# Optimization experiments

Measured on AMD Instinct MI355X. Metric: run time of the kernel, lower is better.

## Reference

```python
import jax, jax.numpy as jnp
import numpy as np

SIZE = 128  # matches init_kwargs output_shape
EPS = 1e-12  # numerical floor for 1 - sum_of_squares (original TF code has none; values stay >0 analytically)


def _chol_from_z(zvec):
    """Build lower-triangular Cholesky factor of a correlation matrix from
    canonical partial-correlation parameters z (|z|<1), per batch row.
    Column j: zeros above, diag = sqrt(1 - s[j]), below-diag = z[i,j]*sqrt(1 - s[i]),
    where s accumulates the row-wise sum of squares of previous columns.
    """
    B = zvec.shape[0]
    n = SIZE
    rows, cols = np.tril_indices(n, -1)  # strictly lower triangle, row-major (matches l_indices)
    z = jnp.zeros((B, n, n), zvec.dtype).at[:, rows, cols].set(zvec)  # [B,n,n]
    i = jnp.arange(n)

    def step(s, xs):
        zcol, j = xs                      # zcol: [B,n] = z[:, :, j]
        sq = jnp.sqrt(jnp.clip(1.0 - s, EPS))  # [B,n] = sqrt(1 - running sum of squares)
        col = jnp.where(i == j, sq, jnp.where(i > j, zcol * sq, 0.0))
        return s + col * col, col

    s0 = jnp.zeros((B, n), zvec.dtype)
    _, cols_out = jax.lax.scan(step, s0, (jnp.moveaxis(z, 2, 0), i))  # cols_out: [n(col), B, n(row)]
    return jnp.transpose(cols_out, (1, 2, 0))  # [B, n, n], L[b, row, col]


def setup_inputs() -> dict:
    key = jax.random.key(0)
    B = 2048
    nz = SIZE * (SIZE - 1) // 2  # 8128
    # canonical partial correlations must lie in (-1, 1)
    zvec = jax.random.uniform(key, (B, nz), jnp.float32, -0.9, 0.9)
    return {"inputs": zvec}


def reference(inputs):
    return _chol_from_z(inputs)
```

## Files before the change

kernel.cpp:

```cpp
#include <hip/hip_runtime.h>

#define NROW 128
#define NZ   8128
#define EPSF 1e-12f
#define RPW  8

typedef float vfloat2 __attribute__((ext_vector_type(2)));

#define DPP_MUL(x, ctrl, rmask)                                               \
  x *= __int_as_float(__builtin_amdgcn_update_dpp(                            \
      0x3f800000, __float_as_int(x), ctrl, rmask, 0xF, false))

__global__ __launch_bounds__(256) void chol_from_z_kernel(
    const float* __restrict__ z, float* __restrict__ out)
{
    const int gtid = blockIdx.x * blockDim.x + threadIdx.x;
    const int w    = gtid >> 6;
    const int lane = threadIdx.x & 63;

    const int row0 = w * RPW;
    const int b    = row0 >> 7;
    const float* __restrict__ zb = z + (size_t)b * NZ;

    const int p0 = lane << 1;
    const int p1 = p0 | 1;

    float zA[RPW], zB[RPW];
    #pragma unroll
    for (int k = 0; k < RPW; ++k) {
        const int i    = (row0 + k) & 127;
        const int base = (i * (i - 1)) >> 1;
        const int ap   = base + p0;
        const int a    = min(ap, NZ - 2);
        const float2 v = *reinterpret_cast<const float2*>(zb + a);
        zA[k] = (ap > a) ? v.y : v.x;
        zB[k] = v.y;
    }

    #pragma unroll
    for (int k = 0; k < RPW; ++k) {
        const int  i  = (row0 + k) & 127;
        const bool m0 = (p0 < i);
        const bool m1 = (p1 < i);
        const float z0 = zA[k], z1 = zB[k];

        const float f0   = m0 ? fmaf(-z0, z0, 1.0f) : 1.0f;
        const float f1   = m1 ? fmaf(-z1, z1, 1.0f) : 1.0f;
        const float pair = f0 * f1;

        float x = pair;
        DPP_MUL(x, 0x111, 0xF);
        DPP_MUL(x, 0x112, 0xF);
        DPP_MUL(x, 0x114, 0xF);
        DPP_MUL(x, 0x118, 0xF);
        DPP_MUL(x, 0x142, 0xA);
        DPP_MUL(x, 0x143, 0xC);

        const float e    = x * __builtin_amdgcn_rcpf(pair);
        const float pre1 = e * f0;

        const float sq0 = __builtin_amdgcn_sqrtf(fmaxf(e,    EPSF));
        const float sq1 = __builtin_amdgcn_sqrtf(fmaxf(pre1, EPSF));

        const float o0 = m0 ? z0 * sq0 : ((p0 == i) ? sq0 : 0.0f);
        const float o1 = m1 ? z1 * sq1 : ((p1 == i) ? sq1 : 0.0f);

        vfloat2 v; v.x = o0; v.y = o1;
        vfloat2* dst = reinterpret_cast<vfloat2*>(out + (size_t)(row0 + k) * NROW + p0);
        __builtin_nontemporal_store(v, dst);
    }
}

extern "C" void kernel_launch(void* const* d_in, const int* in_sizes, int n_in,
                              void* d_out, int out_size, void* d_ws, size_t ws_size,
                              hipStream_t stream)
{
    const float* z = (const float*)d_in[0];
    float* out = (float*)d_out;

    const int B = in_sizes[0] / NZ;
    const int nrows_total = B * NROW;
    const int nwaves = nrows_total / RPW;

    const int block = 256;
    const int grid = (nwaves * 64) / block;
    chol_from_z_kernel<<<grid, block, 0, stream>>>(z, out);
}
```

Baseline: 36.06 us.

## Process four row-units per wave with double-buffered software-pipelined loads

Each wave now handles four 8-row units spaced a grid stride apart instead of one. Loads for the next unit are issued before the current unit is computed and stored, ping-ponging between two register buffers so memory latency overlaps compute. Launch bounds now request 8 waves per EU, and the grid is a quarter of its former size. This raises register pressure and cuts the number of resident waves available to hide latency.

```diff
diff --git a/kernel.cpp b/kernel.cpp
--- a/kernel.cpp
+++ b/kernel.cpp
@@ -11,21 +11,12 @@
   x *= __int_as_float(__builtin_amdgcn_update_dpp(                            \
       0x3f800000, __float_as_int(x), ctrl, rmask, 0xF, false))
 
-__global__ __launch_bounds__(256) void chol_from_z_kernel(
-    const float* __restrict__ z, float* __restrict__ out)
+__device__ __forceinline__ void load_unit(const float* __restrict__ z, int unit,
+                                          int p0, float* zA, float* zB)
 {
-    const int gtid = blockIdx.x * blockDim.x + threadIdx.x;
-    const int w    = gtid >> 6;
-    const int lane = threadIdx.x & 63;
-
-    const int row0 = w * RPW;
+    const int row0 = unit * RPW;
     const int b    = row0 >> 7;
     const float* __restrict__ zb = z + (size_t)b * NZ;
-
-    const int p0 = lane << 1;
-    const int p1 = p0 | 1;
-
-    float zA[RPW], zB[RPW];
     #pragma unroll
     for (int k = 0; k < RPW; ++k) {
         const int i    = (row0 + k) & 127;
@@ -36,7 +27,13 @@
         zA[k] = (ap > a) ? v.y : v.x;
         zB[k] = v.y;
     }
+}
 
+__device__ __forceinline__ void comp_unit(float* __restrict__ out, int unit,
+                                          int p0, int p1,
+                                          const float* zA, const float* zB)
+{
+    const int row0 = unit * RPW;
     #pragma unroll
     for (int k = 0; k < RPW; ++k) {
         const int  i  = (row0 + k) & 127;
@@ -71,6 +68,27 @@
     }
 }
 
+__global__ __launch_bounds__(256, 8) void chol_from_z_kernel(
+    const float* __restrict__ z, float* __restrict__ out, int gw)
+{
+    const int gtid = blockIdx.x * blockDim.x + threadIdx.x;
+    const int w    = gtid >> 6;
+    const int lane = threadIdx.x & 63;
+    const int p0   = lane << 1;
+    const int p1   = p0 | 1;
+
+    float a0[RPW], b0[RPW], a1[RPW], b1[RPW];
+
+    load_unit(z, w,          p0, a0, b0);
+    load_unit(z, w + gw,     p0, a1, b1);
+    comp_unit(out, w,        p0, p1, a0, b0);
+    load_unit(z, w + 2 * gw, p0, a0, b0);
+    comp_unit(out, w + gw,   p0, p1, a1, b1);
+    load_unit(z, w + 3 * gw, p0, a1, b1);
+    comp_unit(out, w + 2*gw, p0, p1, a0, b0);
+    comp_unit(out, w + 3*gw, p0, p1, a1, b1);
+}
+
 extern "C" void kernel_launch(void* const* d_in, const int* in_sizes, int n_in,
                               void* d_out, int out_size, void* d_ws, size_t ws_size,
                               hipStream_t stream)
@@ -79,10 +97,8 @@
     float* out = (float*)d_out;
 
     const int B = in_sizes[0] / NZ;
-    const int nrows_total = B * NROW;
-    const int nwaves = nrows_total / RPW;
-
-    const int block = 256;
-    const int grid = (nwaves * 64) / block;
-    chol_from_z_kernel<<<grid, block, 0, stream>>>(z, out);
+    const int nunits = B * NROW / RPW;
+    const int gw = nunits / 4;
+    const int grid = gw / 4;
+    chol_from_z_kernel<<<grid, 256, 0, stream>>>(z, out, gw);
 }
```

Measured after the change: 37.21 us. +3.2%, slower.
